# Kernel optimization log

Measured on AMD Instinct MI355X. Metric: run time of the kernel, lower is better.

## Reference

```python
import jax, jax.numpy as jnp
import numpy as np
from jax import lax

DIST_THRESH = 180.0
ATT_THRESH = 0.05


def setup_inputs() -> dict:
    key = jax.random.key(0)
    ks = jax.random.split(key, 6)
    B, N, H, W = 16, 512, 25, 25
    F, Fh = H * W, int(H * W * 1.5)  # 625, 937
    x4 = jax.random.normal(ks[0], (B, N, H, W), dtype=jnp.float32) * 0.25
    attention = jax.random.uniform(ks[1], (B, N, 1, 1), dtype=jnp.float32)
    W1 = jax.random.normal(ks[2], (2, F, Fh), dtype=jnp.float32) * (1.0 / np.sqrt(F))
    b1 = jnp.zeros((Fh,), dtype=jnp.float32)
    W2 = jax.random.normal(ks[3], (2, Fh, F), dtype=jnp.float32) * (1.0 / np.sqrt(Fh))
    b2 = jnp.zeros((F,), dtype=jnp.float32)
    return {"x4": x4, "attention": attention, "W1": W1, "b1": b1, "W2": W2, "b2": b2}


def _build_adjacency(X, att):
    """X: [B,N,F] node features, att: [B,N]. Returns thresholded adjacency [B,N,N]."""
    B, N, F = X.shape
    # pairwise L1 distances, row-by-row scan to avoid materializing [B,N,N,F]
    Xs = jnp.swapaxes(X, 0, 1)  # [N,B,F]

    def row(_, xi):  # xi: [B,F]
        d = jnp.sum(jnp.abs(xi[:, None, :] - X), axis=-1)  # [B,N]
        return None, d

    _, D = lax.scan(row, None, Xs)          # [N,B,N]
    D = jnp.swapaxes(D, 0, 1)               # [B,N,N]
    att_d = jnp.abs(att[:, :, None] - att[:, None, :])  # [B,N,N]
    A = ((D <= DIST_THRESH) & (att_d <= ATT_THRESH)).astype(jnp.float32)
    # original only fills i<j and j<i, diagonal stays 0
    A = A * (1.0 - jnp.eye(N, dtype=jnp.float32))
    return A


def _process_graph(A):
    """A + I, then row-normalize by inverse degree (D^-1 (A+I))."""
    N = A.shape[1]
    A = A + jnp.eye(N, dtype=A.dtype)
    deg = jnp.sum(A, axis=-1)               # [B,N]
    dinv = jnp.where(deg > 0, 1.0 / deg, 0.0)
    return dinv[:, :, None] * A


def _cheb_conv(x, L, Wk, b):
    """ChebConv with K=2 over dense normalized graph L: T0=x, T1=Lx."""
    t1 = jnp.einsum('bij,bjf->bif', L, x)
    return jnp.einsum('bnf,fo->bno', x, Wk[0]) + jnp.einsum('bnf,fo->bno', t1, Wk[1]) + b


def reference(x4, attention, W1, b1, W2, b2):
    B, N, H, W = x4.shape
    X = x4.reshape(B, N, H * W)             # [B,N,625] flow_x
    att = attention[:, :, 0, 0]             # [B,N]
    A = _build_adjacency(X, att)
    L = _process_graph(A)
    h = jax.nn.relu(_cheb_conv(X, L, W1, b1))   # [B,N,937]
    out = jax.nn.relu(_cheb_conv(h, L, W2, b2))  # [B,N,625]
    return out
```

## Files before the change

kernel.cpp:

```cpp
#include <hip/hip_runtime.h>
#include <stdint.h>

typedef uint16_t u16;
typedef __attribute__((ext_vector_type(4))) float f32x4;
typedef __attribute__((ext_vector_type(4))) unsigned short us4;
typedef __attribute__((ext_vector_type(8))) unsigned short us8;

#define NB   16
#define NN   512
#define FF   625
#define FH   937
#define ROWS 8192
#define KS1  1280
#define KS2  1920
#define NP1  1024
#define NP2  640
#define F4   160

using frag_ab = __attribute__((ext_vector_type(8))) short;
using frag_cd = __attribute__((ext_vector_type(4))) float;

__device__ __forceinline__ u16 f32_bf16(float f) {
  union { float f; uint32_t u; } x; x.f = f;
  uint32_t r = x.u + 0x7fffu + ((x.u >> 16) & 1u);
  return (u16)(r >> 16);
}
__device__ __forceinline__ float bf16_f32(u16 u) {
  union { uint32_t u; float f; } x; x.u = ((uint32_t)u) << 16;
  return x.f;
}
__device__ __forceinline__ void gload_lds16(const void* g, void* l) {
  __builtin_amdgcn_global_load_lds((__attribute__((address_space(1))) void*)g,
                                   (__attribute__((address_space(3))) void*)l,
                                   16, 0, 0);
}
__device__ __forceinline__ int swiz_row(int blk) {
  return ((blk & 7) << 10) | (blk >> 3);
}

__global__ __launch_bounds__(256) void pad_x(const float* __restrict__ x4,
                                             f32x4* __restrict__ Xpad,
                                             u16* __restrict__ Xcat) {
  const int idx = blockIdx.x * 256 + threadIdx.x;
  if (idx >= ROWS * F4) return;
  const int row = idx / F4;
  const int k4 = idx - row * F4;
  f32x4 v;
  us4 o;
  #pragma unroll
  for (int t = 0; t < 4; ++t) {
    const int f = k4 * 4 + t;
    float x = (f < FF) ? x4[(size_t)row * FF + f] : 0.f;
    v[t] = x;
    o[t] = f32_bf16(x);
  }
  Xpad[idx] = v;
  *(us4*)(Xcat + (size_t)row * KS1 + k4 * 4) = o;
}

__global__ __launch_bounds__(256) void build_graph(
    const f32x4* __restrict__ Xpad,
    const float* __restrict__ att,
    u16* __restrict__ Xcat,
    u16* __restrict__ nbr,
    int* __restrict__ degbuf,
    float* __restrict__ invbuf)
{
  __shared__ float att_sh[512];
  __shared__ f32x4 Xi4[F4];
  __shared__ u16 cand[512];
  __shared__ u16 accj[512];
  __shared__ f32x4 wsum[4][F4];
  __shared__ int ncand, nacc;

  const int tid = threadIdx.x;
  const int row = swiz_row(blockIdx.x);
  const int b = row >> 9;
  const int i = row & 511;
  const f32x4* Xb4 = Xpad + (size_t)b * NN * F4;

  att_sh[tid]       = att[b * NN + tid];
  att_sh[tid + 256] = att[b * NN + tid + 256];
  if (tid < F4) Xi4[tid] = Xb4[(size_t)i * F4 + tid];
  if (tid == 0) { ncand = 0; nacc = 0; }
  __syncthreads();

  const float ai = att_sh[i];
  for (int j = tid; j < NN; j += 256) {
    if (j != i && fabsf(ai - att_sh[j]) <= 0.05f) {
      int p = atomicAdd(&ncand, 1);
      cand[p] = (u16)j;
    }
  }
  __syncthreads();

  const int lane = tid & 63;
  const int wave = tid >> 6;
  const int nc = ncand;

  const f32x4 zero = {0.f, 0.f, 0.f, 0.f};
  f32x4 a0 = Xi4[lane];
  f32x4 a1 = Xi4[64 + lane];
  f32x4 a2 = (lane < 32) ? Xi4[128 + lane] : zero;
  f32x4 s0 = zero, s1 = zero, s2 = zero;

  for (int c = wave; c < nc; c += 4) {
    const int j = cand[c];
    const f32x4* Xj = Xb4 + (size_t)j * F4;
    f32x4 x0 = Xj[lane];
    f32x4 x1 = Xj[64 + lane];
    f32x4 x2 = (lane < 32) ? Xj[128 + lane] : zero;
    f32x4 d0 = a0 - x0, d1 = a1 - x1, d2 = a2 - x2;
    float p = 0.f;
    #pragma unroll
    for (int t = 0; t < 4; ++t)
      p += fabsf(d0[t]) + fabsf(d1[t]) + fabsf(d2[t]);
    #pragma unroll
    for (int off = 32; off; off >>= 1) p += __shfl_xor(p, off, 64);
    if (p <= 180.0f) {
      s0 += x0; s1 += x1; s2 += x2;
      if (lane == 0) { int q = atomicAdd(&nacc, 1); accj[q] = (u16)j; }
    }
  }
  wsum[wave][lane] = s0;
  wsum[wave][64 + lane] = s1;
  if (lane < 32) wsum[wave][128 + lane] = s2;
  __syncthreads();

  const int na = nacc;
  const float inv = 1.0f / (float)(na + 1);
  for (int c = tid; c < na; c += 256) nbr[(size_t)row * 512 + c] = accj[c];
  if (tid == 0) { degbuf[row] = na; invbuf[row] = inv; }

  for (int k = tid; k < F4; k += 256) {
    f32x4 t = Xi4[k];
    #pragma unroll
    for (int w = 0; w < 4; ++w) t += wsum[w][k];
    us4 o;
    #pragma unroll
    for (int s = 0; s < 4; ++s) o[s] = f32_bf16(t[s] * inv);
    *(us4*)(Xcat + (size_t)row * KS1 + 640 + k * 4) = o;
  }
}

__global__ __launch_bounds__(256) void gather2(
    u16* __restrict__ hcat,
    const u16* __restrict__ nbr,
    const int* __restrict__ degbuf,
    const float* __restrict__ invbuf)
{
  __shared__ u16 accj[512];
  __shared__ float hsum[2][8][120];

  const int tid = threadIdx.x;
  const int row = swiz_row(blockIdx.x);
  const int b = row >> 9;
  const int na = degbuf[row];
  const float inv = invbuf[row];
  for (int c = tid; c < na; c += 256) accj[c] = nbr[(size_t)row * 512 + c];
  __syncthreads();

  const int g = tid >> 7;
  const int slot = tid & 127;
  const u16* hbat = hcat + (size_t)b * NN * KS2;

  float s[8] = {0,0,0,0,0,0,0,0};
  if (slot < 120) {
    for (int c = g; c < na; c += 2) {
      const us8 hv = *(const us8*)(hbat + (size_t)accj[c] * KS2 + slot * 8);
      #pragma unroll
      for (int t = 0; t < 8; ++t) s[t] += bf16_f32(hv[t]);
    }
    #pragma unroll
    for (int t = 0; t < 8; ++t) hsum[g][t][slot] = s[t];
  }
  __syncthreads();

  if (tid < 23) hcat[(size_t)row * KS2 + FH + tid] = 0;

  const u16* hrow = hcat + (size_t)row * KS2;
  for (int k = tid; k < 120; k += 256) {
    const us8 hv = *(const us8*)(hrow + k * 8);
    us8 o;
    #pragma unroll
    for (int t = 0; t < 8; ++t) {
      const int col = k * 8 + t;
      float v = (bf16_f32(hv[t]) + hsum[0][t][k] + hsum[1][t][k]) * inv;
      o[t] = (col < FH) ? f32_bf16(v) : (u16)0;
    }
    *(us8*)(hcat + (size_t)row * KS2 + 960 + k * 8) = o;
  }
}

__global__ __launch_bounds__(256) void convert_w1(const float* __restrict__ W1,
                                                  u16* __restrict__ Wt) {
  __shared__ float tile[32][33];
  const int kt = blockIdx.x, nt = blockIdx.y;
  const int tx = threadIdx.x & 31, ty = threadIdx.x >> 5;
  #pragma unroll
  for (int r = 0; r < 4; ++r) {
    int k = kt * 32 + ty + r * 8;
    int n = nt * 32 + tx;
    float v = 0.f;
    int c = -1, kk = 0;
    if (k < 625) { c = 0; kk = k; }
    else if (k >= 640 && k < 1265) { c = 1; kk = k - 640; }
    if (c >= 0 && n < FH) v = W1[((size_t)c * 625 + kk) * FH + n];
    tile[ty + r * 8][tx] = v;
  }
  __syncthreads();
  #pragma unroll
  for (int r = 0; r < 4; ++r) {
    int n = nt * 32 + ty + r * 8;
    int k = kt * 32 + tx;
    Wt[(size_t)n * KS1 + k] = f32_bf16(tile[tx][ty + r * 8]);
  }
}

__global__ __launch_bounds__(256) void convert_w2(const float* __restrict__ W2,
                                                  u16* __restrict__ Wt) {
  __shared__ float tile[32][33];
  const int kt = blockIdx.x, nt = blockIdx.y;
  const int tx = threadIdx.x & 31, ty = threadIdx.x >> 5;
  #pragma unroll
  for (int r = 0; r < 4; ++r) {
    int k = kt * 32 + ty + r * 8;
    int n = nt * 32 + tx;
    float v = 0.f;
    int c = -1, kk = 0;
    if (k < 937) { c = 0; kk = k; }
    else if (k >= 960 && k < 1897) { c = 1; kk = k - 960; }
    if (c >= 0 && n < FF) v = W2[((size_t)c * 937 + kk) * FF + n];
    tile[ty + r * 8][tx] = v;
  }
  __syncthreads();
  #pragma unroll
  for (int r = 0; r < 4; ++r) {
    int n = nt * 32 + ty + r * 8;
    int k = kt * 32 + tx;
    Wt[(size_t)n * KS2 + k] = f32_bf16(tile[tx][ty + r * 8]);
  }
}

template <int KS, int NREAL, int LDC, bool OUT_BF16>
__global__ __launch_bounds__(256) void gemm_bt(
    const u16* __restrict__ A, const u16* __restrict__ Bt,
    const float* __restrict__ bias, void* __restrict__ C)
{
  __shared__ __align__(16) u16 Ash[128 * 32];
  __shared__ __align__(16) u16 Bsh[128 * 32];

  const int tid  = threadIdx.x;
  const int lane = tid & 63;
  const int wave = tid >> 6;
  const int wm = wave & 1, wn = wave >> 1;
  const int q = lane >> 4, l16 = lane & 15;
  const int m0 = blockIdx.x * 128;
  const int n0 = blockIdx.y * 128;

  const int i0 = tid, i1 = 256 + tid;
  const u16* pa0 = A + (size_t)(m0 + (i0 >> 2)) * KS + (i0 & 3) * 8;
  const u16* pa1 = A + (size_t)(m0 + (i1 >> 2)) * KS + (i1 & 3) * 8;
  const u16* pb0 = Bt + (size_t)(n0 + (i0 >> 2)) * KS + (i0 & 3) * 8;
  const u16* pb1 = Bt + (size_t)(n0 + (i1 >> 2)) * KS + (i1 & 3) * 8;
  const int wbase = (tid & 192) * 8;
  u16* la0 = &Ash[wbase];       u16* la1 = &Ash[2048 + wbase];
  u16* lb0 = &Bsh[wbase];       u16* lb1 = &Bsh[2048 + wbase];

  const frag_ab* fA[4]; const frag_ab* fB[4];
  #pragma unroll
  for (int mi = 0; mi < 4; ++mi)
    fA[mi] = (const frag_ab*)&Ash[(wm * 64 + mi * 16 + l16) * 32 + q * 8];
  #pragma unroll
  for (int ni = 0; ni < 4; ++ni)
    fB[ni] = (const frag_ab*)&Bsh[(wn * 64 + ni * 16 + l16) * 32 + q * 8];

  frag_cd acc[4][4] = {};

  constexpr int KT = KS / 32;
  for (int kt = 0; kt < KT; ++kt) {
    __syncthreads();
    gload_lds16(pa0, la0); gload_lds16(pa1, la1);
    gload_lds16(pb0, lb0); gload_lds16(pb1, lb1);
    pa0 += 32; pa1 += 32; pb0 += 32; pb1 += 32;
    __syncthreads();

    frag_ab av[4], bv[4];
    #pragma unroll
    for (int mi = 0; mi < 4; ++mi) av[mi] = *fA[mi];
    #pragma unroll
    for (int ni = 0; ni < 4; ++ni) bv[ni] = *fB[ni];
    #pragma unroll
    for (int mi = 0; mi < 4; ++mi)
      #pragma unroll
      for (int ni = 0; ni < 4; ++ni)
        acc[mi][ni] = __builtin_amdgcn_mfma_f32_16x16x32_bf16(
            av[mi], bv[ni], acc[mi][ni], 0, 0, 0);
  }

  #pragma unroll
  for (int ni = 0; ni < 4; ++ni) {
    const int col = n0 + wn * 64 + ni * 16 + l16;
    const bool ok = (col < NREAL);
    const float bvv = ok ? bias[col] : 0.f;
    #pragma unroll
    for (int mi = 0; mi < 4; ++mi) {
      #pragma unroll
      for (int r = 0; r < 4; ++r) {
        const int rowg = m0 + wm * 64 + mi * 16 + q * 4 + r;
        float v = acc[mi][ni][r] + bvv;
        v = fmaxf(v, 0.f);
        if (ok) {
          if (OUT_BF16)
            ((u16*)C)[(size_t)rowg * LDC + col] = f32_bf16(v);
          else
            ((float*)C)[(size_t)rowg * LDC + col] = v;
        }
      }
    }
  }
}

extern "C" void kernel_launch(void* const* d_in, const int* in_sizes, int n_in,
                              void* d_out, int out_size, void* d_ws, size_t ws_size,
                              hipStream_t stream) {
  const float* x4  = (const float*)d_in[0];
  const float* att = (const float*)d_in[1];
  const float* W1  = (const float*)d_in[2];
  const float* b1  = (const float*)d_in[3];
  const float* W2  = (const float*)d_in[4];
  const float* b2  = (const float*)d_in[5];
  float* out = (float*)d_out;

  char* ws = (char*)d_ws;
  f32x4* Xpad = (f32x4*)ws; ws += (size_t)ROWS * F4 * 16;
  u16* Xcat = (u16*)ws;  ws += (size_t)ROWS * KS1 * 2;
  u16* hcat = (u16*)ws;  ws += (size_t)ROWS * KS2 * 2;
  u16* W1t  = (u16*)ws;  ws += (size_t)NP1 * KS1 * 2;
  u16* W2t  = (u16*)ws;  ws += (size_t)NP2 * KS2 * 2;
  u16* nbr  = (u16*)ws;  ws += (size_t)ROWS * 512 * 2;
  int*   deg = (int*)ws;   ws += (size_t)ROWS * 4;
  float* inv = (float*)ws; ws += (size_t)ROWS * 4;

  convert_w1<<<dim3(KS1 / 32, NP1 / 32), 256, 0, stream>>>(W1, W1t);
  convert_w2<<<dim3(KS2 / 32, NP2 / 32), 256, 0, stream>>>(W2, W2t);
  pad_x<<<dim3((ROWS * F4 + 255) / 256), 256, 0, stream>>>(x4, Xpad, Xcat);
  build_graph<<<dim3(ROWS), 256, 0, stream>>>(Xpad, att, Xcat, nbr, deg, inv);
  gemm_bt<KS1, FH, KS2, true><<<dim3(64, NP1 / 128), 256, 0, stream>>>(
      Xcat, W1t, b1, (void*)hcat);
  gather2<<<dim3(ROWS), 256, 0, stream>>>(hcat, nbr, deg, inv);
  gemm_bt<KS2, FF, FF, false><<<dim3(64, NP2 / 128), 256, 0, stream>>>(
      hcat, W2t, b2, (void*)out);
}
```

Before: 258.6 us.

## Merge prep kernels into one launch and deepen GEMM K-tile with XOR swizzle

Fuses the x padding and both weight transpose/convert kernels into a single launch, with block ranges dispatching to each job, to cut launch overhead. The GEMM now stages 64-wide K tiles instead of 32, halving the number of barrier pairs per output tile. It also applies an XOR swizzle on the 16-byte chunk positions in LDS so that fragment reads avoid bank conflicts. The larger LDS footprint (32KB per block) may reduce occupancy.

```diff
diff --git a/kernel.cpp b/kernel.cpp
--- a/kernel.cpp
+++ b/kernel.cpp
@@ -38,24 +38,73 @@
   return ((blk & 7) << 10) | (blk >> 3);
 }
 
-__global__ __launch_bounds__(256) void pad_x(const float* __restrict__ x4,
-                                             f32x4* __restrict__ Xpad,
-                                             u16* __restrict__ Xcat) {
-  const int idx = blockIdx.x * 256 + threadIdx.x;
-  if (idx >= ROWS * F4) return;
-  const int row = idx / F4;
-  const int k4 = idx - row * F4;
-  f32x4 v;
-  us4 o;
-  #pragma unroll
-  for (int t = 0; t < 4; ++t) {
-    const int f = k4 * 4 + t;
-    float x = (f < FF) ? x4[(size_t)row * FF + f] : 0.f;
-    v[t] = x;
-    o[t] = f32_bf16(x);
-  }
-  Xpad[idx] = v;
-  *(us4*)(Xcat + (size_t)row * KS1 + k4 * 4) = o;
+__global__ __launch_bounds__(256) void prep(
+    const float* __restrict__ x4, const float* __restrict__ W1,
+    const float* __restrict__ W2, f32x4* __restrict__ Xpad,
+    u16* __restrict__ Xcat, u16* __restrict__ W1t, u16* __restrict__ W2t)
+{
+  const int blk = blockIdx.x;
+  if (blk < 5120) {
+    const int idx = blk * 256 + threadIdx.x;
+    if (idx >= ROWS * F4) return;
+    const int row = idx / F4;
+    const int k4 = idx - row * F4;
+    f32x4 v; us4 o;
+    #pragma unroll
+    for (int t = 0; t < 4; ++t) {
+      const int f = k4 * 4 + t;
+      float x = (f < FF) ? x4[(size_t)row * FF + f] : 0.f;
+      v[t] = x; o[t] = f32_bf16(x);
+    }
+    Xpad[idx] = v;
+    *(us4*)(Xcat + (size_t)row * KS1 + k4 * 4) = o;
+  } else if (blk < 6400) {
+    __shared__ float tile[32][33];
+    const int bb = blk - 5120;
+    const int kt = bb % 40, nt = bb / 40;
+    const int tx = threadIdx.x & 31, ty = threadIdx.x >> 5;
+    #pragma unroll
+    for (int r = 0; r < 4; ++r) {
+      int k = kt * 32 + ty + r * 8;
+      int n = nt * 32 + tx;
+      float v = 0.f;
+      int c = -1, kk = 0;
+      if (k < 625) { c = 0; kk = k; }
+      else if (k >= 640 && k < 1265) { c = 1; kk = k - 640; }
+      if (c >= 0 && n < FH) v = W1[((size_t)c * 625 + kk) * FH + n];
+      tile[ty + r * 8][tx] = v;
+    }
+    __syncthreads();
+    #pragma unroll
+    for (int r = 0; r < 4; ++r) {
+      int n = nt * 32 + ty + r * 8;
+      int k = kt * 32 + tx;
+      W1t[(size_t)n * KS1 + k] = f32_bf16(tile[tx][ty + r * 8]);
+    }
+  } else {
+    __shared__ float tile[32][33];
+    const int bb = blk - 6400;
+    const int kt = bb % 60, nt = bb / 60;
+    const int tx = threadIdx.x & 31, ty = threadIdx.x >> 5;
+    #pragma unroll
+    for (int r = 0; r < 4; ++r) {
+      int k = kt * 32 + ty + r * 8;
+      int n = nt * 32 + tx;
+      float v = 0.f;
+      int c = -1, kk = 0;
+      if (k < 937) { c = 0; kk = k; }
+      else if (k >= 960 && k < 1897) { c = 1; kk = k - 960; }
+      if (c >= 0 && n < FF) v = W2[((size_t)c * 937 + kk) * FF + n];
+      tile[ty + r * 8][tx] = v;
+    }
+    __syncthreads();
+    #pragma unroll
+    for (int r = 0; r < 4; ++r) {
+      int n = nt * 32 + ty + r * 8;
+      int k = kt * 32 + tx;
+      W2t[(size_t)n * KS2 + k] = f32_bf16(tile[tx][ty + r * 8]);
+    }
+  }
 }
 
 __global__ __launch_bounds__(256) void build_graph(
@@ -192,63 +241,13 @@
   }
 }
 
-__global__ __launch_bounds__(256) void convert_w1(const float* __restrict__ W1,
-                                                  u16* __restrict__ Wt) {
-  __shared__ float tile[32][33];
-  const int kt = blockIdx.x, nt = blockIdx.y;
-  const int tx = threadIdx.x & 31, ty = threadIdx.x >> 5;
-  #pragma unroll
-  for (int r = 0; r < 4; ++r) {
-    int k = kt * 32 + ty + r * 8;
-    int n = nt * 32 + tx;
-    float v = 0.f;
-    int c = -1, kk = 0;
-    if (k < 625) { c = 0; kk = k; }
-    else if (k >= 640 && k < 1265) { c = 1; kk = k - 640; }
-    if (c >= 0 && n < FH) v = W1[((size_t)c * 625 + kk) * FH + n];
-    tile[ty + r * 8][tx] = v;
-  }
-  __syncthreads();
-  #pragma unroll
-  for (int r = 0; r < 4; ++r) {
-    int n = nt * 32 + ty + r * 8;
-    int k = kt * 32 + tx;
-    Wt[(size_t)n * KS1 + k] = f32_bf16(tile[tx][ty + r * 8]);
-  }
-}
-
-__global__ __launch_bounds__(256) void convert_w2(const float* __restrict__ W2,
-                                                  u16* __restrict__ Wt) {
-  __shared__ float tile[32][33];
-  const int kt = blockIdx.x, nt = blockIdx.y;
-  const int tx = threadIdx.x & 31, ty = threadIdx.x >> 5;
-  #pragma unroll
-  for (int r = 0; r < 4; ++r) {
-    int k = kt * 32 + ty + r * 8;
-    int n = nt * 32 + tx;
-    float v = 0.f;
-    int c = -1, kk = 0;
-    if (k < 937) { c = 0; kk = k; }
-    else if (k >= 960 && k < 1897) { c = 1; kk = k - 960; }
-    if (c >= 0 && n < FF) v = W2[((size_t)c * 937 + kk) * FF + n];
-    tile[ty + r * 8][tx] = v;
-  }
-  __syncthreads();
-  #pragma unroll
-  for (int r = 0; r < 4; ++r) {
-    int n = nt * 32 + ty + r * 8;
-    int k = kt * 32 + tx;
-    Wt[(size_t)n * KS2 + k] = f32_bf16(tile[tx][ty + r * 8]);
-  }
-}
-
 template <int KS, int NREAL, int LDC, bool OUT_BF16>
-__global__ __launch_bounds__(256) void gemm_bt(
+__global__ __launch_bounds__(256) void gemm_bt64(
     const u16* __restrict__ A, const u16* __restrict__ Bt,
     const float* __restrict__ bias, void* __restrict__ C)
 {
-  __shared__ __align__(16) u16 Ash[128 * 32];
-  __shared__ __align__(16) u16 Bsh[128 * 32];
+  __shared__ __align__(16) u16 Ash[128 * 64];
+  __shared__ __align__(16) u16 Bsh[128 * 64];
 
   const int tid  = threadIdx.x;
   const int lane = tid & 63;
@@ -258,44 +257,58 @@
   const int m0 = blockIdx.x * 128;
   const int n0 = blockIdx.y * 128;
 
-  const int i0 = tid, i1 = 256 + tid;
-  const u16* pa0 = A + (size_t)(m0 + (i0 >> 2)) * KS + (i0 & 3) * 8;
-  const u16* pa1 = A + (size_t)(m0 + (i1 >> 2)) * KS + (i1 & 3) * 8;
-  const u16* pb0 = Bt + (size_t)(n0 + (i0 >> 2)) * KS + (i0 & 3) * 8;
-  const u16* pb1 = Bt + (size_t)(n0 + (i1 >> 2)) * KS + (i1 & 3) * 8;
+  const u16* pa[4]; const u16* pb[4];
+  #pragma unroll
+  for (int r = 0; r < 4; ++r) {
+    const int ci = r * 256 + tid;
+    const int row = ci >> 3, cpos = ci & 7;
+    const int csrc = cpos ^ (row & 7);
+    pa[r] = A  + (size_t)(m0 + row) * KS + csrc * 8;
+    pb[r] = Bt + (size_t)(n0 + row) * KS + csrc * 8;
+  }
   const int wbase = (tid & 192) * 8;
-  u16* la0 = &Ash[wbase];       u16* la1 = &Ash[2048 + wbase];
-  u16* lb0 = &Bsh[wbase];       u16* lb1 = &Bsh[2048 + wbase];
-
-  const frag_ab* fA[4]; const frag_ab* fB[4];
+
+  const frag_ab* fA[4][2]; const frag_ab* fB[4][2];
   #pragma unroll
-  for (int mi = 0; mi < 4; ++mi)
-    fA[mi] = (const frag_ab*)&Ash[(wm * 64 + mi * 16 + l16) * 32 + q * 8];
+  for (int mi = 0; mi < 4; ++mi) {
+    const int row = wm * 64 + mi * 16 + l16;
+    fA[mi][0] = (const frag_ab*)&Ash[row * 64 + ((q    ) ^ (l16 & 7)) * 8];
+    fA[mi][1] = (const frag_ab*)&Ash[row * 64 + ((q + 4) ^ (l16 & 7)) * 8];
+  }
   #pragma unroll
-  for (int ni = 0; ni < 4; ++ni)
-    fB[ni] = (const frag_ab*)&Bsh[(wn * 64 + ni * 16 + l16) * 32 + q * 8];
+  for (int ni = 0; ni < 4; ++ni) {
+    const int row = wn * 64 + ni * 16 + l16;
+    fB[ni][0] = (const frag_ab*)&Bsh[row * 64 + ((q    ) ^ (l16 & 7)) * 8];
+    fB[ni][1] = (const frag_ab*)&Bsh[row * 64 + ((q + 4) ^ (l16 & 7)) * 8];
+  }
 
   frag_cd acc[4][4] = {};
 
-  constexpr int KT = KS / 32;
+  constexpr int KT = KS / 64;
   for (int kt = 0; kt < KT; ++kt) {
     __syncthreads();
-    gload_lds16(pa0, la0); gload_lds16(pa1, la1);
-    gload_lds16(pb0, lb0); gload_lds16(pb1, lb1);
-    pa0 += 32; pa1 += 32; pb0 += 32; pb1 += 32;
+    #pragma unroll
+    for (int r = 0; r < 4; ++r) {
+      gload_lds16(pa[r], &Ash[r * 2048 + wbase]);
+      gload_lds16(pb[r], &Bsh[r * 2048 + wbase]);
+      pa[r] += 64; pb[r] += 64;
+    }
     __syncthreads();
 
-    frag_ab av[4], bv[4];
-    #pragma unroll
-    for (int mi = 0; mi < 4; ++mi) av[mi] = *fA[mi];
-    #pragma unroll
-    for (int ni = 0; ni < 4; ++ni) bv[ni] = *fB[ni];
-    #pragma unroll
-    for (int mi = 0; mi < 4; ++mi)
-      #pragma unroll
-      for (int ni = 0; ni < 4; ++ni)
-        acc[mi][ni] = __builtin_amdgcn_mfma_f32_16x16x32_bf16(
-            av[mi], bv[ni], acc[mi][ni], 0, 0, 0);
+    #pragma unroll
+    for (int kk = 0; kk < 2; ++kk) {
+      frag_ab av[4], bv[4];
+      #pragma unroll
+      for (int mi = 0; mi < 4; ++mi) av[mi] = *fA[mi][kk];
+      #pragma unroll
+      for (int ni = 0; ni < 4; ++ni) bv[ni] = *fB[ni][kk];
+      #pragma unroll
+      for (int mi = 0; mi < 4; ++mi)
+        #pragma unroll
+        for (int ni = 0; ni < 4; ++ni)
+          acc[mi][ni] = __builtin_amdgcn_mfma_f32_16x16x32_bf16(
+              av[mi], bv[ni], acc[mi][ni], 0, 0, 0);
+    }
   }
 
   #pragma unroll
@@ -342,13 +355,11 @@
   int*   deg = (int*)ws;   ws += (size_t)ROWS * 4;
   float* inv = (float*)ws; ws += (size_t)ROWS * 4;
 
-  convert_w1<<<dim3(KS1 / 32, NP1 / 32), 256, 0, stream>>>(W1, W1t);
-  convert_w2<<<dim3(KS2 / 32, NP2 / 32), 256, 0, stream>>>(W2, W2t);
-  pad_x<<<dim3((ROWS * F4 + 255) / 256), 256, 0, stream>>>(x4, Xpad, Xcat);
+  prep<<<dim3(7600), 256, 0, stream>>>(x4, W1, W2, Xpad, Xcat, W1t, W2t);
   build_graph<<<dim3(ROWS), 256, 0, stream>>>(Xpad, att, Xcat, nbr, deg, inv);
-  gemm_bt<KS1, FH, KS2, true><<<dim3(64, NP1 / 128), 256, 0, stream>>>(
+  gemm_bt64<KS1, FH, KS2, true><<<dim3(64, NP1 / 128), 256, 0, stream>>>(
       Xcat, W1t, b1, (void*)hcat);
   gather2<<<dim3(ROWS), 256, 0, stream>>>(hcat, nbr, deg, inv);
-  gemm_bt<KS2, FF, FF, false><<<dim3(64, NP2 / 128), 256, 0, stream>>>(
+  gemm_bt64<KS2, FF, FF, false><<<dim3(64, NP2 / 128), 256, 0, stream>>>(
       hcat, W2t, b2, (void*)out);
 }
```

Result: faster. 244.3 us (-5.5%).
